# Kernel tuning notes

Measured on AMD Instinct MI355X. Metric: run time of the kernel, lower is better.

Reference implementation:

```python
import jax, jax.numpy as jnp
import numpy as np
import math

B, C, T = 4, 512, 2048
H = 8            # num_heads
G = 32           # GroupNorm groups (GroupNorm32 in ADM-style code)
EPS = 1e-5


def setup_inputs() -> dict:
    key = jax.random.key(0)
    ks = jax.random.split(key, 7)
    x = jax.random.normal(ks[0], (B, C, T), jnp.float32)
    norm_scale = 1.0 + 0.02 * jax.random.normal(ks[1], (C,), jnp.float32)
    norm_bias = 0.02 * jax.random.normal(ks[2], (C,), jnp.float32)
    qkv_w = 0.02 * jax.random.normal(ks[3], (3 * C, C), jnp.float32)  # 1x1 conv == matmul
    qkv_b = 0.02 * jax.random.normal(ks[4], (3 * C,), jnp.float32)
    proj_w = 0.02 * jax.random.normal(ks[5], (C, C), jnp.float32)
    proj_b = 0.02 * jax.random.normal(ks[6], (C,), jnp.float32)
    return {"x": x, "norm_scale": norm_scale, "norm_bias": norm_bias,
            "qkv_w": qkv_w, "qkv_b": qkv_b, "proj_w": proj_w, "proj_b": proj_b}


def _group_norm(x, scale, bias):
    # x: [B, C, T]; 32-group norm over (C/G, T) per group
    b, c, t = x.shape
    xg = x.reshape(b, G, (c // G) * t)
    mean = jnp.mean(xg, axis=-1, keepdims=True)
    var = jnp.var(xg, axis=-1, keepdims=True)
    xg = (xg - mean) * jax.lax.rsqrt(var + EPS)
    return xg.reshape(b, c, t) * scale[None, :, None] + bias[None, :, None]


def reference(x, norm_scale, norm_bias, qkv_w, qkv_b, proj_w, proj_b):
    b, c, t = x.shape
    ch = c // H
    h = _group_norm(x, norm_scale, norm_bias)
    qkv = jnp.einsum('oc,bct->bot', qkv_w, h) + qkv_b[None, :, None]  # [B, 3C, T]
    q, k, v = jnp.split(qkv, 3, axis=1)
    q = q.reshape(b * H, ch, t)
    k = k.reshape(b * H, ch, t)
    v = v.reshape(b * H, ch, t)
    scale = 1.0 / math.sqrt(math.sqrt(ch))
    w = jnp.einsum('bct,bcs->bts', q * scale, k * scale)              # [B*H, T, T]
    w = jax.nn.softmax(w.astype(jnp.float32), axis=-1).astype(qkv.dtype)
    a = jnp.einsum('bts,bcs->bct', w, v).reshape(b, c, t)             # [B, C, T]
    out = jnp.einsum('oc,bct->bot', proj_w, a) + proj_b[None, :, None]
    return x + out
```

## Files before the change

kernel.cpp:

```cpp
#include <hip/hip_runtime.h>

typedef short bf16x8 __attribute__((ext_vector_type(8)));
typedef float f32x4 __attribute__((ext_vector_type(4)));
typedef float f32x16 __attribute__((ext_vector_type(16)));
typedef unsigned short u16;
typedef unsigned int u32;

constexpr int B = 4, C = 512, T = 2048, H = 8, G = 32;
constexpr int CH = C / H;
constexpr int CPG = C / G;
constexpr float EPS = 1e-5f;
constexpr float SCLQ = 0.18033688011112042f;

__device__ __forceinline__ u16 f2bf(float f) {
  union { float f; u32 u; } v; v.f = f;
  return (u16)((v.u + 0x7FFFu + ((v.u >> 16) & 1u)) >> 16);
}

__device__ __forceinline__ void gload16(const void* g, void* lds) {
  __builtin_amdgcn_global_load_lds(
      (const __attribute__((address_space(1))) void*)g,
      (__attribute__((address_space(3))) void*)lds, 16, 0, 0);
}

__device__ __forceinline__ void pl32swap(u32& a, u32& b) {
  asm("v_permlane32_swap_b32 %0, %1" : "+v"(a), "+v"(b));
}

template <int ROWS>
__device__ __forceinline__ void stage_swz_4w(u16* lds, const u16* gsrc, int ldk) {
  const int tid = threadIdx.x;
  const int w = tid >> 6, lane = tid & 63;
#pragma unroll
  for (int i = 0; i < ROWS / 32; ++i) {
    const int chunk = i * 4 + w;
    const int row = chunk * 8 + (lane >> 3);
    const int col = ((lane & 7) * 8) ^ ((row & 7) << 3);
    gload16(gsrc + (size_t)row * ldk + col, (char*)lds + chunk * 1024);
  }
}

template <int ROWS>
__device__ __forceinline__ void stage_swz_8w(u16* lds, const u16* gsrc, int ldk) {
  const int tid = threadIdx.x;
  const int w = tid >> 6, lane = tid & 63;
#pragma unroll
  for (int i = 0; i < ROWS / 64; ++i) {
    const int chunk = i * 8 + w;
    const int row = chunk * 8 + (lane >> 3);
    const int col = ((lane & 7) * 8) ^ ((row & 7) << 3);
    gload16(gsrc + (size_t)row * ldk + col, (char*)lds + chunk * 1024);
  }
}

__global__ __launch_bounds__(256) void prep_k(const float* __restrict__ x,
                                              float* __restrict__ stats,
                                              const float* __restrict__ s1,
                                              u16* __restrict__ d1, int n1,
                                              const float* __restrict__ s2,
                                              u16* __restrict__ d2, int n2) {
  __shared__ float red[8];
  const int bid = blockIdx.x;
  if (bid < 1024) {
    int i = bid * 256 + threadIdx.x;
    const float4* src = (const float4*)s1;
    uint2* dst = (uint2*)d1;
    if (i >= n1) { i -= n1; if (i >= n2) return; src = (const float4*)s2; dst = (uint2*)d2; }
    float4 v = src[i];
    uint2 pk;
    pk.x = (u32)f2bf(v.x) | ((u32)f2bf(v.y) << 16);
    pk.y = (u32)f2bf(v.z) | ((u32)f2bf(v.w) << 16);
    dst[i] = pk;
    return;
  }
  const int bg = bid - 1024;
  const float4* xp = (const float4*)(x + (size_t)bg * CPG * T);
  float s = 0.f, ss = 0.f;
  for (int i = threadIdx.x; i < CPG * T / 4; i += 256) {
    float4 v = xp[i];
    s += v.x + v.y + v.z + v.w;
    ss += v.x * v.x + v.y * v.y + v.z * v.z + v.w * v.w;
  }
  for (int off = 32; off; off >>= 1) {
    s += __shfl_down(s, off);
    ss += __shfl_down(ss, off);
  }
  const int w = threadIdx.x >> 6;
  if ((threadIdx.x & 63) == 0) { red[w] = s; red[4 + w] = ss; }
  __syncthreads();
  if (threadIdx.x == 0) {
    float S = red[0] + red[1] + red[2] + red[3];
    float SS = red[4] + red[5] + red[6] + red[7];
    const float inv = 1.f / (float)(CPG * T);
    float mean = S * inv;
    float var = SS * inv - mean * mean;
    stats[bg * 2] = mean;
    stats[bg * 2 + 1] = rsqrtf(var + EPS);
  }
}

__global__ __launch_bounds__(256) void gn_apply_k(const float* __restrict__ x,
                                                  const float* __restrict__ stats,
                                                  const float* __restrict__ gsc,
                                                  const float* __restrict__ gbi,
                                                  u16* __restrict__ ht) {
  const int b = blockIdx.y;
  const int t0 = blockIdx.x * 32;
#pragma unroll
  for (int p = 0; p < 2; ++p) {
    const int c = p * 256 + threadIdx.x;
    const int bg = b * G + (c >> 4);
    const float mean = stats[bg * 2], rstd = stats[bg * 2 + 1];
    const float sc = gsc[c] * rstd;
    const float bi = gbi[c] - mean * sc;
    const float4* xp = (const float4*)(x + ((size_t)b * C + c) * T + t0);
#pragma unroll
    for (int j = 0; j < 8; ++j) {
      float4 v = xp[j];
      const int t = t0 + j * 4;
      u16* hp = ht + ((size_t)b * T + t) * C + c;
      hp[0]     = f2bf(v.x * sc + bi);
      hp[C]     = f2bf(v.y * sc + bi);
      hp[2 * C] = f2bf(v.z * sc + bi);
      hp[3 * C] = f2bf(v.w * sc + bi);
    }
  }
}

__global__ __launch_bounds__(256) void qkv_gemm_k(const u16* __restrict__ ht,
                                                  const u16* __restrict__ wq,
                                                  const float* __restrict__ qkvb,
                                                  u16* __restrict__ qo,
                                                  u16* __restrict__ kvo_k,
                                                  u16* __restrict__ kvo_v) {
  __shared__ u16 As[128 * 64];
  __shared__ u16 Bs[128 * 64];
  const int bid = blockIdx.x;
  const int wg = (bid & 7) * 96 + (bid >> 3);
  const int nt = wg % 12;
  const int mtb = wg / 12;
  const int mt = mtb & 15, b = mtb >> 4;
  const u16* Ab = ht + ((size_t)b * T + mt * 128) * C;
  const u16* Bb = wq + (size_t)nt * 128 * C;
  const int tid = threadIdx.x, lane = tid & 63, w = tid >> 6;
  const int wr = w >> 1, wc = w & 1, l15 = lane & 15, lhi = lane >> 4;
  const int swz = (l15 & 7) << 3;

  const f32x4 vzero = {0.f, 0.f, 0.f, 0.f};
  f32x4 acc[4][4];
#pragma unroll
  for (int m = 0; m < 4; ++m)
#pragma unroll
    for (int n = 0; n < 4; ++n) acc[m][n] = vzero;

  for (int kt = 0; kt < C / 64; ++kt) {
    stage_swz_4w<128>(As, Ab + kt * 64, C);
    stage_swz_4w<128>(Bs, Bb + kt * 64, C);
    __syncthreads();
#pragma unroll
    for (int kk = 0; kk < 2; ++kk) {
      const int koff = (kk * 32 + lhi * 8) ^ swz;
      bf16x8 af[4], bfv[4];
#pragma unroll
      for (int m = 0; m < 4; ++m)
        af[m] = *(const bf16x8*)&As[(wr * 64 + m * 16 + l15) * 64 + koff];
#pragma unroll
      for (int n = 0; n < 4; ++n)
        bfv[n] = *(const bf16x8*)&Bs[(wc * 64 + n * 16 + l15) * 64 + koff];
#pragma unroll
      for (int m = 0; m < 4; ++m)
#pragma unroll
        for (int n = 0; n < 4; ++n)
          acc[m][n] = __builtin_amdgcn_mfma_f32_16x16x32_bf16(af[m], bfv[n], acc[m][n], 0, 0, 0);
    }
    __syncthreads();
  }
#pragma unroll
  for (int n = 0; n < 4; ++n) {
    const int o = nt * 128 + wc * 64 + n * 16 + l15;
    const float bias = qkvb[o];
    const int which = o >> 9, rem = o & 511, hh = rem >> 6, d = rem & 63;
    const size_t bh = (size_t)b * H + hh;
#pragma unroll
    for (int m = 0; m < 4; ++m) {
      const int tbase = mt * 128 + wr * 64 + m * 16 + lhi * 4;
#pragma unroll
      for (int r = 0; r < 4; ++r) {
        float val = acc[m][n][r] + bias;
        if (which == 0) val *= SCLQ;
        const u16 bv = f2bf(val);
        const int t = tbase + r;
        if (which == 0)      qo[(bh * T + t) * CH + d] = bv;
        else if (which == 1) kvo_k[(bh * T + t) * CH + d] = bv;
        else                 kvo_v[(bh * CH + d) * T + t] = bv;
      }
    }
  }
}

__global__ __launch_bounds__(512, 4) void attn_k(const u16* __restrict__ q,
                                                 const u16* __restrict__ k,
                                                 const u16* __restrict__ v,
                                                 u16* __restrict__ at) {
  __shared__ u16 Ks[2][128 * 64];
  __shared__ u16 Vs[2][2][64 * 64];
  const int lin = blockIdx.x + (blockIdx.y << 4);
  const int wg = (lin & 7) * 64 + (lin >> 3);
  const int qt = wg & 15, bh = wg >> 4;
  const int tid = threadIdx.x, lane = tid & 63, w = tid >> 6;
  const int qset = w & 3, grp = w >> 2;
  const int l31 = lane & 31, h = lane >> 5;
  const u16* qb = q + (size_t)bh * T * CH;
  const u16* kb = k + (size_t)bh * T * CH;
  const u16* vb = v + (size_t)bh * CH * T;
  constexpr int NP = T / 128;

  bf16x8 qf[4];
  {
    const u16* qp = qb + (size_t)(qt * 128 + qset * 32 + l31) * CH + h * 8;
#pragma unroll
    for (int ks = 0; ks < 4; ++ks) qf[ks] = *(const bf16x8*)(qp + ks * 16);
  }
  union { u32 u[4]; bf16x8 v8; } ones;
#pragma unroll
  for (int i = 0; i < 4; ++i) ones.u[i] = 0x3F803F80u;

  stage_swz_8w<128>(Ks[0], kb, CH);
  stage_swz_8w<64>(Vs[0][0], vb, T);
  stage_swz_8w<64>(Vs[0][1], vb + 64, T);
  asm volatile("s_waitcnt vmcnt(0)" ::: "memory");
  __builtin_amdgcn_s_barrier();
  asm volatile("" ::: "memory");

  f32x16 accO0 = {0.f,0.f,0.f,0.f,0.f,0.f,0.f,0.f,0.f,0.f,0.f,0.f,0.f,0.f,0.f,0.f};
  f32x16 accO1 = accO0;
  f32x16 accL = accO0;
  const int kswz = (l31 & 7) << 3;

  int cur = 0;
  for (int p = 0; p < NP; ++p) {
    if (p + 1 < NP) {
      stage_swz_8w<128>(Ks[cur ^ 1], kb + (size_t)(p + 1) * 128 * CH, CH);
      stage_swz_8w<64>(Vs[cur ^ 1][0], vb + (p + 1) * 128, T);
      stage_swz_8w<64>(Vs[cur ^ 1][1], vb + (p + 1) * 128 + 64, T);
    }
    const u16* Kc = &Ks[cur][grp * 64 * 64];
    const u16* Vc = Vs[cur][grp];

    f32x16 accS0 = {0.f,0.f,0.f,0.f,0.f,0.f,0.f,0.f,0.f,0.f,0.f,0.f,0.f,0.f,0.f,0.f};
    f32x16 accS1 = accS0;
    __builtin_amdgcn_s_setprio(1);
#pragma unroll
    for (int ks = 0; ks < 4; ++ks) {
      const int col = (ks * 16 + h * 8) ^ kswz;
      bf16x8 kf0 = *(const bf16x8*)&Kc[l31 * 64 + col];
      bf16x8 kf1 = *(const bf16x8*)&Kc[(32 + l31) * 64 + col];
      accS0 = __builtin_amdgcn_mfma_f32_32x32x16_bf16(kf0, qf[ks], accS0, 0, 0, 0);
      accS1 = __builtin_amdgcn_mfma_f32_32x32x16_bf16(kf1, qf[ks], accS1, 0, 0, 0);
    }
    __builtin_amdgcn_s_setprio(0);

    u32 wd0[8], wd1[8];
#pragma unroll
    for (int i = 0; i < 8; ++i) {
      float pa = __builtin_amdgcn_exp2f(accS0[2 * i]);
      float pb = __builtin_amdgcn_exp2f(accS0[2 * i + 1]);
      asm("v_cvt_pk_bf16_f32 %0, %1, %2" : "=v"(wd0[i]) : "v"(pa), "v"(pb));
    }
#pragma unroll
    for (int i = 0; i < 8; ++i) {
      float pa = __builtin_amdgcn_exp2f(accS1[2 * i]);
      float pb = __builtin_amdgcn_exp2f(accS1[2 * i + 1]);
      asm("v_cvt_pk_bf16_f32 %0, %1, %2" : "=v"(wd1[i]) : "v"(pa), "v"(pb));
    }
    pl32swap(wd0[0], wd0[2]); pl32swap(wd0[1], wd0[3]);
    pl32swap(wd0[4], wd0[6]); pl32swap(wd0[5], wd0[7]);
    pl32swap(wd1[0], wd1[2]); pl32swap(wd1[1], wd1[3]);
    pl32swap(wd1[4], wd1[6]); pl32swap(wd1[5], wd1[7]);

    __builtin_amdgcn_s_setprio(1);
#pragma unroll
    for (int kt = 0; kt < 2; ++kt) {
      const u32* wd = kt ? wd1 : wd0;
      union { u32 u[4]; bf16x8 v8; } fa, fb;
      fa.u[0] = wd[0]; fa.u[1] = wd[1]; fa.u[2] = wd[2]; fa.u[3] = wd[3];
      fb.u[0] = wd[4]; fb.u[1] = wd[5]; fb.u[2] = wd[6]; fb.u[3] = wd[7];
      const int sA = (kt * 32 + h * 8) ^ kswz;
      const int sB = (kt * 32 + 16 + h * 8) ^ kswz;
      {
        bf16x8 vf0 = *(const bf16x8*)&Vc[l31 * 64 + sA];
        bf16x8 vf1 = *(const bf16x8*)&Vc[l31 * 64 + sB];
        accO0 = __builtin_amdgcn_mfma_f32_32x32x16_bf16(fa.v8, vf0, accO0, 0, 0, 0);
        accO0 = __builtin_amdgcn_mfma_f32_32x32x16_bf16(fb.v8, vf1, accO0, 0, 0, 0);
      }
      {
        bf16x8 vf0 = *(const bf16x8*)&Vc[(32 + l31) * 64 + sA];
        bf16x8 vf1 = *(const bf16x8*)&Vc[(32 + l31) * 64 + sB];
        accO1 = __builtin_amdgcn_mfma_f32_32x32x16_bf16(fa.v8, vf0, accO1, 0, 0, 0);
        accO1 = __builtin_amdgcn_mfma_f32_32x32x16_bf16(fb.v8, vf1, accO1, 0, 0, 0);
      }
      accL = __builtin_amdgcn_mfma_f32_32x32x16_bf16(fa.v8, ones.v8, accL, 0, 0, 0);
      accL = __builtin_amdgcn_mfma_f32_32x32x16_bf16(fb.v8, ones.v8, accL, 0, 0, 0);
    }
    __builtin_amdgcn_s_setprio(0);

    asm volatile("s_waitcnt vmcnt(0)" ::: "memory");
    __builtin_amdgcn_s_barrier();
    asm volatile("" ::: "memory");
    cur ^= 1;
  }

  float* fO = (float*)&Ks[0][0];
  float* fL = (float*)&Vs[0][0][0];
  if (grp == 1) {
#pragma unroll
    for (int r = 0; r < 16; ++r) {
      const int qrow = (r & 3) + 8 * (r >> 2) + 4 * h;
      float* row = fO + (qset * 32 + qrow) * 64;
      row[l31] = accO0[r];
      row[32 + l31] = accO1[r];
      if (l31 == 0) fL[qset * 32 + qrow] = accL[r];
    }
  }
  __syncthreads();
  if (grp == 0) {
    const int bq = bh >> 3, hh = bh & 7;
#pragma unroll
    for (int r = 0; r < 16; ++r) {
      const int qrow = (r & 3) + 8 * (r >> 2) + 4 * h;
      const float denom = accL[r] + fL[qset * 32 + qrow];
      const float invr = __builtin_amdgcn_rcpf(denom);
      const float* row = fO + (qset * 32 + qrow) * 64;
      const float o0 = accO0[r] + row[l31];
      const float o1 = accO1[r] + row[32 + l31];
      const int t = qt * 128 + qset * 32 + qrow;
      u16* op = at + ((size_t)bq * T + t) * C + hh * 64 + l31;
      op[0]  = f2bf(o0 * invr);
      op[32] = f2bf(o1 * invr);
    }
  }
}

__global__ __launch_bounds__(256) void proj_gemm_k(const u16* __restrict__ at,
                                                   const u16* __restrict__ wp,
                                                   const float* __restrict__ pb,
                                                   const float* __restrict__ x,
                                                   float* __restrict__ out) {
  __shared__ u16 As[128 * 64];
  __shared__ u16 Bs[128 * 64];
  const int bid = blockIdx.x;
  const int wg = (bid & 7) * 32 + (bid >> 3);
  const int nt = wg & 3;
  const int mtb = wg >> 2;
  const int mt = mtb & 15, b = mtb >> 4;
  const u16* Ab = at + ((size_t)b * T + mt * 128) * C;
  const u16* Bb = wp + (size_t)nt * 128 * C;
  const int tid = threadIdx.x, lane = tid & 63, w = tid >> 6;
  const int wr = w >> 1, wc = w & 1, l15 = lane & 15, lhi = lane >> 4;
  const int swz = (l15 & 7) << 3;

  const f32x4 vzero = {0.f, 0.f, 0.f, 0.f};
  f32x4 acc[4][4];
#pragma unroll
  for (int m = 0; m < 4; ++m)
#pragma unroll
    for (int n = 0; n < 4; ++n) acc[m][n] = vzero;

  for (int kt = 0; kt < C / 64; ++kt) {
    stage_swz_4w<128>(As, Ab + kt * 64, C);
    stage_swz_4w<128>(Bs, Bb + kt * 64, C);
    __syncthreads();
#pragma unroll
    for (int kk = 0; kk < 2; ++kk) {
      const int koff = (kk * 32 + lhi * 8) ^ swz;
      bf16x8 af[4], bfv[4];
#pragma unroll
      for (int m = 0; m < 4; ++m)
        af[m] = *(const bf16x8*)&As[(wr * 64 + m * 16 + l15) * 64 + koff];
#pragma unroll
      for (int n = 0; n < 4; ++n)
        bfv[n] = *(const bf16x8*)&Bs[(wc * 64 + n * 16 + l15) * 64 + koff];
#pragma unroll
      for (int m = 0; m < 4; ++m)
#pragma unroll
        for (int n = 0; n < 4; ++n)
          acc[m][n] = __builtin_amdgcn_mfma_f32_16x16x32_bf16(af[m], bfv[n], acc[m][n], 0, 0, 0);
    }
    __syncthreads();
  }
#pragma unroll
  for (int n = 0; n < 4; ++n) {
    const int o = nt * 128 + wc * 64 + n * 16 + l15;
    const float bias = pb[o];
#pragma unroll
    for (int m = 0; m < 4; ++m) {
      const int tbase = mt * 128 + wr * 64 + m * 16 + lhi * 4;
#pragma unroll
      for (int r = 0; r < 4; ++r) {
        const int t = tbase + r;
        const size_t idx = ((size_t)b * C + o) * T + t;
        out[idx] = x[idx] + acc[m][n][r] + bias;
      }
    }
  }
}

extern "C" void kernel_launch(void* const* d_in, const int* in_sizes, int n_in,
                              void* d_out, int out_size, void* d_ws, size_t ws_size,
                              hipStream_t stream) {
  const float* x     = (const float*)d_in[0];
  const float* gsc   = (const float*)d_in[1];
  const float* gbi   = (const float*)d_in[2];
  const float* qkvw  = (const float*)d_in[3];
  const float* qkvb  = (const float*)d_in[4];
  const float* projw = (const float*)d_in[5];
  const float* projb = (const float*)d_in[6];
  float* out = (float*)d_out;

  char* ws = (char*)d_ws;
  float* stats = (float*)ws;
  u16* wq = (u16*)(ws + 1024);
  u16* wp = (u16*)(ws + 1024 + 1572864);
  u16* ht = (u16*)(ws + 2098176);
  u16* qo = (u16*)(ws + 10486784);
  u16* ko = (u16*)(ws + 18875392);
  u16* vo = (u16*)(ws + 27264000);
  u16* at = ht;

  prep_k<<<1152, 256, 0, stream>>>(x, stats, qkvw, wq, 196608, projw, wp, 65536);
  gn_apply_k<<<dim3(T / 32, B), 256, 0, stream>>>(x, stats, gsc, gbi, ht);
  qkv_gemm_k<<<768, 256, 0, stream>>>(ht, wq, qkvb, qo, ko, vo);
  attn_k<<<dim3(T / 128, B * H), 512, 0, stream>>>(qo, ko, vo, at);
  proj_gemm_k<<<256, 256, 0, stream>>>(at, wp, projb, x, out);
}
```

Before: 120.4 us.

## Use 8-wave blocks in QKV and proj GEMMs and halve proj N-tile

The QKV GEMM now runs 512-thread blocks (8 waves) over the same 128x128 tile, so each wave computes a 32x64 sub-tile instead of 64x64. The projection GEMM moves to 128x64 tiles with 512 blocks of 8 waves, each wave owning a 16x64 strip. The aim is more waves per tile, to hide latency better and to fill the CUs with the small proj grid. The cost is less reuse of each LDS fragment load per MFMA, and more B-tile reloads for proj. The code relies on a stage_swz_8w helper assumed to exist in the hidden part of the file.

```diff
diff --git a/kernel.cpp b/kernel.cpp
--- a/kernel.cpp
+++ b/kernel.cpp
@@ -127,12 +127,12 @@
   }
 }
 
-__global__ __launch_bounds__(256) void qkv_gemm_k(const u16* __restrict__ ht,
-                                                  const u16* __restrict__ wq,
-                                                  const float* __restrict__ qkvb,
-                                                  u16* __restrict__ qo,
-                                                  u16* __restrict__ kvo_k,
-                                                  u16* __restrict__ kvo_v) {
+__global__ __launch_bounds__(512, 2) void qkv_gemm_k(const u16* __restrict__ ht,
+                                                     const u16* __restrict__ wq,
+                                                     const float* __restrict__ qkvb,
+                                                     u16* __restrict__ qo,
+                                                     u16* __restrict__ kvo_k,
+                                                     u16* __restrict__ kvo_v) {
   __shared__ u16 As[128 * 64];
   __shared__ u16 Bs[128 * 64];
   const int bid = blockIdx.x;
@@ -147,28 +147,28 @@
   const int swz = (l15 & 7) << 3;
 
   const f32x4 vzero = {0.f, 0.f, 0.f, 0.f};
-  f32x4 acc[4][4];
-#pragma unroll
-  for (int m = 0; m < 4; ++m)
+  f32x4 acc[2][4];
+#pragma unroll
+  for (int m = 0; m < 2; ++m)
 #pragma unroll
     for (int n = 0; n < 4; ++n) acc[m][n] = vzero;
 
   for (int kt = 0; kt < C / 64; ++kt) {
-    stage_swz_4w<128>(As, Ab + kt * 64, C);
-    stage_swz_4w<128>(Bs, Bb + kt * 64, C);
+    stage_swz_8w<128>(As, Ab + kt * 64, C);
+    stage_swz_8w<128>(Bs, Bb + kt * 64, C);
     __syncthreads();
 #pragma unroll
     for (int kk = 0; kk < 2; ++kk) {
       const int koff = (kk * 32 + lhi * 8) ^ swz;
-      bf16x8 af[4], bfv[4];
-#pragma unroll
-      for (int m = 0; m < 4; ++m)
-        af[m] = *(const bf16x8*)&As[(wr * 64 + m * 16 + l15) * 64 + koff];
+      bf16x8 af[2], bfv[4];
+#pragma unroll
+      for (int m = 0; m < 2; ++m)
+        af[m] = *(const bf16x8*)&As[(wr * 32 + m * 16 + l15) * 64 + koff];
 #pragma unroll
       for (int n = 0; n < 4; ++n)
         bfv[n] = *(const bf16x8*)&Bs[(wc * 64 + n * 16 + l15) * 64 + koff];
 #pragma unroll
-      for (int m = 0; m < 4; ++m)
+      for (int m = 0; m < 2; ++m)
 #pragma unroll
         for (int n = 0; n < 4; ++n)
           acc[m][n] = __builtin_amdgcn_mfma_f32_16x16x32_bf16(af[m], bfv[n], acc[m][n], 0, 0, 0);
@@ -182,8 +182,8 @@
     const int which = o >> 9, rem = o & 511, hh = rem >> 6, d = rem & 63;
     const size_t bh = (size_t)b * H + hh;
 #pragma unroll
-    for (int m = 0; m < 4; ++m) {
-      const int tbase = mt * 128 + wr * 64 + m * 16 + lhi * 4;
+    for (int m = 0; m < 2; ++m) {
+      const int tbase = mt * 128 + wr * 32 + m * 16 + lhi * 4;
 #pragma unroll
       for (int r = 0; r < 4; ++r) {
         float val = acc[m][n][r] + bias;
@@ -341,66 +341,57 @@
   }
 }
 
-__global__ __launch_bounds__(256) void proj_gemm_k(const u16* __restrict__ at,
-                                                   const u16* __restrict__ wp,
-                                                   const float* __restrict__ pb,
-                                                   const float* __restrict__ x,
-                                                   float* __restrict__ out) {
+__global__ __launch_bounds__(512, 2) void proj_gemm_k(const u16* __restrict__ at,
+                                                      const u16* __restrict__ wp,
+                                                      const float* __restrict__ pb,
+                                                      const float* __restrict__ x,
+                                                      float* __restrict__ out) {
   __shared__ u16 As[128 * 64];
-  __shared__ u16 Bs[128 * 64];
+  __shared__ u16 Bs[64 * 64];
   const int bid = blockIdx.x;
-  const int wg = (bid & 7) * 32 + (bid >> 3);
-  const int nt = wg & 3;
-  const int mtb = wg >> 2;
+  const int wg = (bid & 7) * 64 + (bid >> 3);
+  const int nt = wg & 7;
+  const int mtb = wg >> 3;
   const int mt = mtb & 15, b = mtb >> 4;
   const u16* Ab = at + ((size_t)b * T + mt * 128) * C;
-  const u16* Bb = wp + (size_t)nt * 128 * C;
+  const u16* Bb = wp + (size_t)nt * 64 * C;
   const int tid = threadIdx.x, lane = tid & 63, w = tid >> 6;
-  const int wr = w >> 1, wc = w & 1, l15 = lane & 15, lhi = lane >> 4;
+  const int l15 = lane & 15, lhi = lane >> 4;
   const int swz = (l15 & 7) << 3;
 
   const f32x4 vzero = {0.f, 0.f, 0.f, 0.f};
-  f32x4 acc[4][4];
-#pragma unroll
-  for (int m = 0; m < 4; ++m)
-#pragma unroll
-    for (int n = 0; n < 4; ++n) acc[m][n] = vzero;
+  f32x4 acc[4];
+#pragma unroll
+  for (int n = 0; n < 4; ++n) acc[n] = vzero;
 
   for (int kt = 0; kt < C / 64; ++kt) {
-    stage_swz_4w<128>(As, Ab + kt * 64, C);
-    stage_swz_4w<128>(Bs, Bb + kt * 64, C);
+    stage_swz_8w<128>(As, Ab + kt * 64, C);
+    stage_swz_8w<64>(Bs, Bb + kt * 64, C);
     __syncthreads();
 #pragma unroll
     for (int kk = 0; kk < 2; ++kk) {
       const int koff = (kk * 32 + lhi * 8) ^ swz;
-      bf16x8 af[4], bfv[4];
-#pragma unroll
-      for (int m = 0; m < 4; ++m)
-        af[m] = *(const bf16x8*)&As[(wr * 64 + m * 16 + l15) * 64 + koff];
+      bf16x8 af = *(const bf16x8*)&As[(w * 16 + l15) * 64 + koff];
+      bf16x8 bfv[4];
 #pragma unroll
       for (int n = 0; n < 4; ++n)
-        bfv[n] = *(const bf16x8*)&Bs[(wc * 64 + n * 16 + l15) * 64 + koff];
-#pragma unroll
-      for (int m = 0; m < 4; ++m)
-#pragma unroll
-        for (int n = 0; n < 4; ++n)
-          acc[m][n] = __builtin_amdgcn_mfma_f32_16x16x32_bf16(af[m], bfv[n], acc[m][n], 0, 0, 0);
+        bfv[n] = *(const bf16x8*)&Bs[(n * 16 + l15) * 64 + koff];
+#pragma unroll
+      for (int n = 0; n < 4; ++n)
+        acc[n] = __builtin_amdgcn_mfma_f32_16x16x32_bf16(af, bfv[n], acc[n], 0, 0, 0);
     }
     __syncthreads();
   }
 #pragma unroll
   for (int n = 0; n < 4; ++n) {
-    const int o = nt * 128 + wc * 64 + n * 16 + l15;
+    const int o = nt * 64 + n * 16 + l15;
     const float bias = pb[o];
-#pragma unroll
-    for (int m = 0; m < 4; ++m) {
-      const int tbase = mt * 128 + wr * 64 + m * 16 + lhi * 4;
-#pragma unroll
-      for (int r = 0; r < 4; ++r) {
-        const int t = tbase + r;
-        const size_t idx = ((size_t)b * C + o) * T + t;
-        out[idx] = x[idx] + acc[m][n][r] + bias;
-      }
+    const int tbase = mt * 128 + w * 16 + lhi * 4;
+#pragma unroll
+    for (int r = 0; r < 4; ++r) {
+      const int t = tbase + r;
+      const size_t idx = ((size_t)b * C + o) * T + t;
+      out[idx] = x[idx] + acc[n][r] + bias;
     }
   }
 }
@@ -429,7 +420,7 @@
 
   prep_k<<<1152, 256, 0, stream>>>(x, stats, qkvw, wq, 196608, projw, wp, 65536);
   gn_apply_k<<<dim3(T / 32, B), 256, 0, stream>>>(x, stats, gsc, gbi, ht);
-  qkv_gemm_k<<<768, 256, 0, stream>>>(ht, wq, qkvb, qo, ko, vo);
+  qkv_gemm_k<<<768, 512, 0, stream>>>(ht, wq, qkvb, qo, ko, vo);
   attn_k<<<dim3(T / 128, B * H), 512, 0, stream>>>(qo, ko, vo, at);
-  proj_gemm_k<<<256, 256, 0, stream>>>(at, wp, projb, x, out);
-}
+  proj_gemm_k<<<512, 512, 0, stream>>>(at, wp, projb, x, out);
+}
```

Result: faster. 114.1 us (-5.3%).
